# Kernel optimization log

Measured on AMD Instinct MI355X. Metric: run time of the kernel, lower is better.

## Reference

```python
import jax, jax.numpy as jnp
import numpy as np

B = 32; NPG = 290; N = B * NPG; EPG = 2320; E = B * EPG
LP = 900; IN_FEATS = 75; D = 128; HD = 256; K = 3; HK = HD * K; HOUT = 2


def setup_inputs() -> dict:
    key = jax.random.key(0)
    ks = jax.random.split(key, 20)
    s = 0.05
    rng = np.random.default_rng(0)
    off = np.arange(B)[:, None] * NPG  # keep edges inside each graph block
    edge_src = jnp.asarray((rng.integers(0, NPG, (B, EPG)) + off).reshape(-1), dtype=jnp.int32)
    edge_dst = jnp.asarray((rng.integers(0, NPG, (B, EPG)) + off).reshape(-1), dtype=jnp.int32)
    node_h = jax.random.normal(ks[0], (N, IN_FEATS), jnp.float32)
    v_p = jax.random.randint(ks[1], (B, LP), 0, 26, jnp.int32)
    W_init = (jax.random.normal(ks[2], (IN_FEATS, D)) * s).at[:, -1].set(0.0)  # padding unit zeroed
    gcn_W = jax.random.normal(ks[3], (3, 3, D, D)) * s
    gcn_b = jnp.zeros((3, 3, D))
    gcn_Wres = jax.random.normal(ks[4], (3, 3, D, D)) * s
    gcn_bres = jnp.zeros((3, 3, D))
    emb = (jax.random.normal(ks[5], (26, D)) * s).at[0].set(0.0)  # padding_idx=0
    conv1_w = jax.random.normal(ks[6], (D, D, 3)) * s
    conv2_w = jax.random.normal(ks[7], (D, D, 6)) * s
    conv3_w = jax.random.normal(ks[8], (D, D, 9)) * s
    conv_b = jnp.zeros((3, D))
    cnn_bn_g = jnp.ones((3, D)); cnn_bn_b = jnp.zeros((3, D))
    Wv = jax.random.normal(ks[9], (D, HK)) * s; bv = jnp.zeros((HK,))
    Wq = jax.random.normal(ks[10], (D, HK)) * s; bq = jnp.zeros((HK,))
    h_mat = jax.random.normal(ks[11], (HOUT, HK)) * s
    h_bias = jnp.zeros((HOUT,))
    ban_bn_g = jnp.ones((HD,)); ban_bn_b = jnp.zeros((HD,))
    m_w1 = jax.random.normal(ks[12], (HD, 512)) * s; m_b1 = jnp.zeros((512,))
    m_w2 = jax.random.normal(ks[13], (512, 512)) * s; m_b2 = jnp.zeros((512,))
    m_w3 = jax.random.normal(ks[14], (512, 128)) * s; m_b3 = jnp.zeros((128,))
    m_w4 = jax.random.normal(ks[15], (128, 1)) * s; m_b4 = jnp.zeros((1,))
    mbn_g1 = jnp.ones((512,)); mbn_b1 = jnp.zeros((512,))
    mbn_g2 = jnp.ones((512,)); mbn_b2 = jnp.zeros((512,))
    mbn_g3 = jnp.ones((128,)); mbn_b3 = jnp.zeros((128,))
    return dict(node_h=node_h, edge_src=edge_src, edge_dst=edge_dst, v_p=v_p,
                W_init=W_init, gcn_W=gcn_W, gcn_b=gcn_b, gcn_Wres=gcn_Wres, gcn_bres=gcn_bres,
                emb=emb, conv1_w=conv1_w, conv2_w=conv2_w, conv3_w=conv3_w, conv_b=conv_b,
                cnn_bn_g=cnn_bn_g, cnn_bn_b=cnn_bn_b, Wv=Wv, bv=bv, Wq=Wq, bq=bq,
                h_mat=h_mat, h_bias=h_bias, ban_bn_g=ban_bn_g, ban_bn_b=ban_bn_b,
                m_w1=m_w1, m_b1=m_b1, m_w2=m_w2, m_b2=m_b2, m_w3=m_w3, m_b3=m_b3,
                m_w4=m_w4, m_b4=m_b4, mbn_g1=mbn_g1, mbn_b1=mbn_b1, mbn_g2=mbn_g2,
                mbn_b2=mbn_b2, mbn_g3=mbn_g3, mbn_b3=mbn_b3)


def _bn_feat(x, g, b):  # BatchNorm1d on [B, C], training-mode batch stats
    m = jnp.mean(x, 0); v = jnp.var(x, 0)
    return (x - m) * jax.lax.rsqrt(v + 1e-5) * g + b


def _bn_chan(x, g, b):  # BatchNorm1d on [B, C, L]
    m = jnp.mean(x, (0, 2), keepdims=True); v = jnp.var(x, (0, 2), keepdims=True)
    return (x - m) * jax.lax.rsqrt(v + 1e-5) * g[None, :, None] + b[None, :, None]


def _forward(node_h, W_init, gcn_W, gcn_b, gcn_Wres, gcn_bres, emb, conv1_w, conv2_w,
             conv3_w, conv_b, cnn_bn_g, cnn_bn_b, Wv, bv, Wq, bq, h_mat, h_bias,
             ban_bn_g, ban_bn_b, m_w1, m_b1, m_w2, m_b2, m_w3, m_b3, m_w4, m_b4,
             mbn_g1, mbn_b1, mbn_g2, mbn_b2, mbn_g3, mbn_b3, edge_src, edge_dst, v_p):
    relu = jax.nn.relu

    def gcn(h, W, b, Wr, br):  # 3 dgllife GCN layers: sum-aggregate + relu + residual
        for l in range(3):
            agg = jax.ops.segment_sum(h[edge_src], edge_dst, num_segments=N)
            h = relu(agg @ W[l] + b[l]) + relu(h @ Wr[l] + br[l])
        return h

    h0 = node_h @ W_init  # shared init_transform (no bias)
    v_d_o = gcn(h0, gcn_W[0], gcn_b[0], gcn_Wres[0], gcn_bres[0]).reshape(B, NPG, D)
    pos1 = gcn(h0, gcn_W[1], gcn_b[1], gcn_Wres[1], gcn_bres[1]).reshape(B, NPG, D)
    pos2 = gcn(h0, gcn_W[2], gcn_b[2], gcn_Wres[2], gcn_bres[2]).reshape(B, NPG, D)

    x = emb[v_p].transpose(0, 2, 1)  # [B, D, LP]
    dn = ('NCH', 'OIH', 'NCH')
    for w, cb, g, bb in ((conv1_w, conv_b[0], cnn_bn_g[0], cnn_bn_b[0]),
                         (conv2_w, conv_b[1], cnn_bn_g[1], cnn_bn_b[1]),
                         (conv3_w, conv_b[2], cnn_bn_g[2], cnn_bn_b[2])):
        x = jax.lax.conv_general_dilated(x, w, (1,), 'VALID', dimension_numbers=dn) + cb[None, :, None]
        x = _bn_chan(relu(x), g, bb)
    v_p_o = x.transpose(0, 2, 1)  # [B, 885, D]

    q_ = relu(v_p_o @ Wq + bq)  # BAN q_net (shared across views)

    def ban(vd):  # BANLayer forward (eval-mode dropout)
        v_ = relu(vd @ Wv + bv)  # [B, Nv, HK]
        att = jnp.einsum('hk,bvk,bqk->bhvq', h_mat, v_, q_) + h_bias[None, :, None, None]
        f = jnp.einsum('bvk,bhvq,bqk->bk', v_, att, q_)  # summed over h_out heads
        f = f.reshape(-1, HD, K).sum(-1)  # AvgPool1d(k) * k == sum over k groups
        return _bn_feat(f, ban_bn_g, ban_bn_b)

    def mlp(f):
        f = _bn_feat(relu(f @ m_w1 + m_b1), mbn_g1, mbn_b1)
        f = _bn_feat(relu(f @ m_w2 + m_b2), mbn_g2, mbn_b2)
        f = _bn_feat(relu(f @ m_w3 + m_b3), mbn_g3, mbn_b3)
        return f @ m_w4 + m_b4

    f_o = ban(v_d_o)  # Transformer_lar treated as identity -> beta blend is a no-op
    score_o = mlp(f_o)
    s1 = mlp(ban(pos1))
    s2 = mlp(ban(pos2))

    def norm(z):
        return z / jnp.maximum(jnp.linalg.norm(z, axis=1, keepdims=True), 1e-12)

    km = norm(s1) @ norm(s2).T  # cosine_similarity_kernel
    loss = -jnp.mean(jnp.diagonal(jax.nn.log_softmax(km, axis=1)))  # CE vs arange labels
    return jnp.concatenate([score_o, s1, s2, loss * jnp.ones((B, 1), score_o.dtype)], axis=1)


def reference(node_h, edge_src, edge_dst, v_p, W_init, gcn_W, gcn_b, gcn_Wres, gcn_bres,
              emb, conv1_w, conv2_w, conv3_w, conv_b, cnn_bn_g, cnn_bn_b, Wv, bv, Wq, bq,
              h_mat, h_bias, ban_bn_g, ban_bn_b, m_w1, m_b1, m_w2, m_b2, m_w3, m_b3,
              m_w4, m_b4, mbn_g1, mbn_b1, mbn_g2, mbn_b2, mbn_g3, mbn_b3):
    return _forward(node_h, W_init, gcn_W, gcn_b, gcn_Wres, gcn_bres, emb, conv1_w,
                    conv2_w, conv3_w, conv_b, cnn_bn_g, cnn_bn_b, Wv, bv, Wq, bq,
                    h_mat, h_bias, ban_bn_g, ban_bn_b, m_w1, m_b1, m_w2, m_b2, m_w3,
                    m_b3, m_w4, m_b4, mbn_g1, mbn_b1, mbn_g2, mbn_b2, mbn_g3, mbn_b3,
                    edge_src, edge_dst, v_p)
```

## Files before the change

kernel.cpp:

```cpp
#include <hip/hip_runtime.h>
#include <hip/hip_bf16.h>

#define Bc 32
#define NPGc 290
#define Nn 9280
#define Ec 74240
#define LPc 900
#define INFc 75
#define Dd 128
#define HKc 768
#define LQ 885
#define S1 904
#define S2 896
#define S3 888
#define NT 78
#define TSZ 4096

typedef __attribute__((ext_vector_type(8))) short bf16x8;
typedef __attribute__((ext_vector_type(16))) float f32x16;

static __device__ __forceinline__ unsigned short f2bf(float v){
  unsigned int u = __float_as_uint(v);
  unsigned int r = u + 0x7FFFu + ((u >> 16) & 1u);
  return (unsigned short)(r >> 16);
}
static __device__ __forceinline__ float bf2f(unsigned short b){
  return __uint_as_float(((unsigned int)b) << 16);
}

__global__ void k_sentinel(float* out, float val){
  int t = threadIdx.x;
  if (t < 128) out[t] = val;
}

__global__ void k_h0(float* __restrict__ h0, const float* __restrict__ nh, const float* __restrict__ Wi){
  int n = blockIdx.x, j = threadIdx.x;
  __shared__ float arow[INFc];
  if (j < INFc) arow[j] = nh[(size_t)n*INFc + j];
  __syncthreads();
  float s = 0.f;
  #pragma unroll 5
  for (int k=0;k<INFc;k++) s += arow[k]*Wi[(size_t)k*Dd + j];
  h0[(size_t)n*Dd + j] = s;
}

__global__ void k_build_adj(float* __restrict__ A, const int* __restrict__ src, const int* __restrict__ dst){
  int e = blockIdx.x*blockDim.x + threadIdx.x;
  if (e >= Ec) return;
  int s = src[e], d = dst[e];
  int b = d / NPGc;
  int dl = d - b*NPGc, sl = s - b*NPGc;
  atomicAdd(&A[((size_t)b*NPGc + dl)*NPGc + sl], 1.f);
}

__global__ void k_wsplit(unsigned short* __restrict__ dstW, unsigned short* __restrict__ dstWr,
                         const float* __restrict__ W, const float* __restrict__ Wr){
  int idx = blockIdx.x*256 + threadIdx.x;
  if (idx >= 9*Dd*Dd) return;
  int gl = idx >> 14;
  int r  = idx & 16383;
  int k  = r >> 7, j = r & 127;
  int c = k >> 4, slot = k & 15;
  size_t o = ((((size_t)gl*8 + c)*Dd + j) << 4) + slot;
  const size_t NW = (size_t)9*8*Dd*16;
  float v = W[idx];
  unsigned short hi = f2bf(v);
  dstW[o] = hi; dstW[NW + o] = f2bf(v - bf2f(hi));
  float u = Wr[idx];
  unsigned short hr = f2bf(u);
  dstWr[o] = hr; dstWr[NW + o] = f2bf(u - bf2f(hr));
}

__global__ void k_aggm(unsigned short* __restrict__ aggH, unsigned short* __restrict__ aggL,
                       const float* __restrict__ inb, size_t istride,
                       const float* __restrict__ Adj){
  int g = blockIdx.z, b = blockIdx.y;
  int i0 = blockIdx.x*64;
  const float* h = inb + (size_t)g*istride + (size_t)b*NPGc*Dd;
  const float* Ab = Adj + (size_t)b*NPGc*NPGc;
  __shared__ unsigned short Bh[128*24], Bl[128*24];
  int tid = threadIdx.x;
  int w = tid>>6, l = tid&63, lr = l&31, lg = l>>5;
  int mh = w>>1, nh = w&1;
  int kr = tid>>4, jq = tid&15;
  f32x16 acc0={}, acc1={};
  for (int c=0;c<19;c++){
    int k0 = c*16;
    {
      int ci = k0 + kr;
      if (ci < NPGc){
        const float* hr_ = h + (size_t)ci*Dd + jq*8;
        #pragma unroll
        for (int m=0;m<8;m++){
          float v = hr_[m];
          unsigned short hi16 = f2bf(v);
          Bh[(jq*8+m)*24 + kr] = hi16;
          Bl[(jq*8+m)*24 + kr] = f2bf(v - bf2f(hi16));
        }
      } else {
        #pragma unroll
        for (int m=0;m<8;m++){ Bh[(jq*8+m)*24+kr]=0; Bl[(jq*8+m)*24+kr]=0; }
      }
    }
    __syncthreads();
    int row = i0 + mh*32 + lr;
    bf16x8 aA = {0,0,0,0,0,0,0,0};
    if (row < NPGc && k0+15 < NPGc){
      const float* ar_ = Ab + (size_t)row*NPGc + k0 + lg*8;
      #pragma unroll
      for (int m=0;m<8;m++) aA[m] = (short)f2bf(ar_[m]);
    } else if (row < NPGc){
      #pragma unroll
      for (int m=0;m<8;m++){
        int k = k0 + lg*8 + m;
        aA[m] = (short)((k < NPGc) ? f2bf(Ab[(size_t)row*NPGc + k]) : 0);
      }
    }
    bf16x8 b0H = *(const bf16x8*)&Bh[(nh*64+lr)*24 + lg*8];
    bf16x8 b0L = *(const bf16x8*)&Bl[(nh*64+lr)*24 + lg*8];
    bf16x8 b1H = *(const bf16x8*)&Bh[(nh*64+32+lr)*24 + lg*8];
    bf16x8 b1L = *(const bf16x8*)&Bl[(nh*64+32+lr)*24 + lg*8];
    acc0 = __builtin_amdgcn_mfma_f32_32x32x16_bf16(aA, b0H, acc0, 0, 0, 0);
    acc0 = __builtin_amdgcn_mfma_f32_32x32x16_bf16(aA, b0L, acc0, 0, 0, 0);
    acc1 = __builtin_amdgcn_mfma_f32_32x32x16_bf16(aA, b1H, acc1, 0, 0, 0);
    acc1 = __builtin_amdgcn_mfma_f32_32x32x16_bf16(aA, b1L, acc1, 0, 0, 0);
    __syncthreads();
  }
  size_t gb = ((size_t)g*Bc + b)*NPGc;
  int j0 = nh*64 + lr;
  #pragma unroll
  for (int reg=0; reg<16; reg++){
    int rowl = (reg&3) + 8*(reg>>2) + 4*lg;
    int i = i0 + mh*32 + rowl;
    if (i < NPGc){
      size_t base = (gb + i)*Dd;
      float v0 = acc0[reg];
      unsigned short h0_ = f2bf(v0);
      aggH[base + j0] = h0_;
      aggL[base + j0] = f2bf(v0 - bf2f(h0_));
      float v1 = acc1[reg];
      unsigned short h1_ = f2bf(v1);
      aggH[base + j0 + 32] = h1_;
      aggL[base + j0 + 32] = f2bf(v1 - bf2f(h1_));
    }
  }
}

__global__ void k_gcnlin(float* __restrict__ outb, size_t ostride,
                         const unsigned short* __restrict__ aggH, const unsigned short* __restrict__ aggL,
                         const float* __restrict__ inb, size_t istride,
                         const unsigned short* __restrict__ WTs, const unsigned short* __restrict__ WrTs,
                         const float* __restrict__ ball, const float* __restrict__ brall, int lno){
  int g = blockIdx.y;
  int m0 = blockIdx.x*64;
  int gl = g*3 + lno;
  const size_t NW = (size_t)9*8*Dd*16;
  int tid = threadIdx.x;
  int w=tid>>6, l=tid&63, lr=l&31, lg=l>>5;
  int mh=w>>1, nh=w&1;
  const float* hin = inb + (size_t)g*istride;
  const unsigned short* agH = aggH + (size_t)g*Nn*Dd;
  const unsigned short* agL = aggL + (size_t)g*Nn*Dd;
  f32x16 aw0={},aw1={},ar0={},ar1={};
  int row = m0 + mh*32 + lr;
  for (int c=0;c<8;c++){
    int k0 = c*16;
    bf16x8 gH = *(const bf16x8*)&agH[(size_t)row*Dd + k0 + lg*8];
    bf16x8 gL = *(const bf16x8*)&agL[(size_t)row*Dd + k0 + lg*8];
    bf16x8 hH, hL;
    {
      const float* hp = hin + (size_t)row*Dd + k0 + lg*8;
      #pragma unroll
      for (int m=0;m<8;m++){
        float v = hp[m];
        unsigned short x = f2bf(v);
        hH[m] = (short)x;
        hL[m] = (short)f2bf(v - bf2f(x));
      }
    }
    size_t wb0 = ((((size_t)gl*8 + c)*Dd) + nh*64 + lr)*16 + (size_t)lg*8;
    size_t wb1 = wb0 + 32*16;
    bf16x8 w0H = *(const bf16x8*)&WTs[wb0];
    bf16x8 w0L = *(const bf16x8*)&WTs[NW + wb0];
    bf16x8 w1H = *(const bf16x8*)&WTs[wb1];
    bf16x8 w1L = *(const bf16x8*)&WTs[NW + wb1];
    bf16x8 r0H = *(const bf16x8*)&WrTs[wb0];
    bf16x8 r0L = *(const bf16x8*)&WrTs[NW + wb0];
    bf16x8 r1H = *(const bf16x8*)&WrTs[wb1];
    bf16x8 r1L = *(const bf16x8*)&WrTs[NW + wb1];
    aw0 = __builtin_amdgcn_mfma_f32_32x32x16_bf16(gH, w0H, aw0, 0,0,0);
    aw0 = __builtin_amdgcn_mfma_f32_32x32x16_bf16(gH, w0L, aw0, 0,0,0);
    aw0 = __builtin_amdgcn_mfma_f32_32x32x16_bf16(gL, w0H, aw0, 0,0,0);
    aw1 = __builtin_amdgcn_mfma_f32_32x32x16_bf16(gH, w1H, aw1, 0,0,0);
    aw1 = __builtin_amdgcn_mfma_f32_32x32x16_bf16(gH, w1L, aw1, 0,0,0);
    aw1 = __builtin_amdgcn_mfma_f32_32x32x16_bf16(gL, w1H, aw1, 0,0,0);
    ar0 = __builtin_amdgcn_mfma_f32_32x32x16_bf16(hH, r0H, ar0, 0,0,0);
    ar0 = __builtin_amdgcn_mfma_f32_32x32x16_bf16(hH, r0L, ar0, 0,0,0);
    ar0 = __builtin_amdgcn_mfma_f32_32x32x16_bf16(hL, r0H, ar0, 0,0,0);
    ar1 = __builtin_amdgcn_mfma_f32_32x32x16_bf16(hH, r1H, ar1, 0,0,0);
    ar1 = __builtin_amdgcn_mfma_f32_32x32x16_bf16(hH, r1L, ar1, 0,0,0);
    ar1 = __builtin_amdgcn_mfma_f32_32x32x16_bf16(hL, r1H, ar1, 0,0,0);
  }
  float* out = outb + (size_t)g*ostride;
  int j0 = nh*64 + lr;
  float b0 = ball[gl*Dd + j0], b1 = ball[gl*Dd + j0 + 32];
  float c0 = brall[gl*Dd + j0], c1 = brall[gl*Dd + j0 + 32];
  #pragma unroll
  for (int reg=0; reg<16; reg++){
    int rowl = (reg&3)+8*(reg>>2)+4*lg;
    int i = m0 + mh*32 + rowl;
    out[(size_t)i*Dd + j0]      = fmaxf(aw0[reg]+b0,0.f) + fmaxf(ar0[reg]+c0,0.f);
    out[(size_t)i*Dd + j0 + 32] = fmaxf(aw1[reg]+b1,0.f) + fmaxf(ar1[reg]+c1,0.f);
  }
}

__global__ void k_embed(float* __restrict__ x, const int* __restrict__ vp, const float* __restrict__ emb){
  int t = blockIdx.x*blockDim.x + threadIdx.x;
  int d = blockIdx.y, b = blockIdx.z;
  if (t >= LPc) return;
  int tok = vp[b*LPc + t];
  x[((size_t)b*Dd + d)*LPc + t] = emb[(size_t)tok*Dd + d];
}

__global__ void k_wpack16(unsigned short* __restrict__ wp, const float* __restrict__ w,
                          const float* __restrict__ scale, int KW, int C){
  int idx = blockIdx.x*256 + threadIdx.x;
  int tot = C*2048;
  if (idx >= tot) return;
  int c = idx >> 11;
  int r = idx & 2047;
  int o = r >> 4, s = r & 15;
  int k = c*16 + s;
  int i = k / KW, kw = k - i*KW;
  float v = w[((size_t)o*Dd + i)*KW + kw];
  if (scale) v *= scale[i];
  unsigned short hi = f2bf(v);
  wp[idx] = hi;
  wp[(size_t)tot + idx] = f2bf(v - bf2f(hi));
}

__global__ void k_bfold(float* __restrict__ bout, const float* __restrict__ w,
                        const float* __restrict__ shf, const float* __restrict__ cb,
                        int go, int KW){
  int o = blockIdx.x, i = threadIdx.x;
  float p = 0.f;
  if (shf){
    const float* wr = w + ((size_t)o*Dd + i)*KW;
    float s = 0.f;
    for (int kw=0; kw<KW; kw++) s += wr[kw];
    p = s * shf[i];
  }
  __shared__ float red[128];
  red[i] = p; __syncthreads();
  for (int st=64; st>0; st>>=1){
    if (i<st) red[i] += red[i+st];
    __syncthreads();
  }
  if (i==0) bout[o] = cb[go+o] + red[0];
}

template<int KW>
__global__ void k_convmfma2(float* __restrict__ y, const float* __restrict__ x,
                            const unsigned short* __restrict__ wp,
                            const float* __restrict__ biasF,
                            int Lout, int XS, int YS){
  const int C = (Dd*KW)/16;
  int b = blockIdx.y;
  int t0 = blockIdx.x*64;
  __shared__ unsigned short Bh[2][64*24], Bl[2][64*24];
  int tid = threadIdx.x;
  int w = tid>>6, l = tid&63, lr = l&31, lg = l>>5;
  int kx = tid&15, tq = tid>>4;
  const unsigned short* wpL = wp + (size_t)C*2048;
  const float* xb = x + (size_t)b*Dd*XS;
  f32x16 acc0={}, acc1={};
  {
    int i = kx/KW, kw = kx - i*KW;
    const float* xr = xb + (size_t)i*XS + t0 + kw + tq*4;
    #pragma unroll
    for (int j=0;j<4;j++){
      float v = xr[j];
      unsigned short h = f2bf(v);
      Bh[0][(tq*4+j)*24+kx] = h;
      Bl[0][(tq*4+j)*24+kx] = f2bf(v - bf2f(h));
    }
  }
  __syncthreads();
  for (int c=0;c<C;c++){
    int cur = c&1, nxt = cur^1;
    bf16x8 aH = *(const bf16x8*)(wp  + ((size_t)c*128 + w*32+lr)*16 + lg*8);
    bf16x8 aL = *(const bf16x8*)(wpL + ((size_t)c*128 + w*32+lr)*16 + lg*8);
    float pv0=0.f,pv1=0.f,pv2=0.f,pv3=0.f;
    if (c+1<C){
      int k1 = (c+1)*16 + kx;
      int i = k1/KW, kw = k1 - i*KW;
      const float* xr = xb + (size_t)i*XS + t0 + kw + tq*4;
      pv0 = xr[0]; pv1 = xr[1]; pv2 = xr[2]; pv3 = xr[3];
    }
    bf16x8 b0H = *(const bf16x8*)&Bh[cur][lr*24 + lg*8];
    bf16x8 b0L = *(const bf16x8*)&Bl[cur][lr*24 + lg*8];
    bf16x8 b1H = *(const bf16x8*)&Bh[cur][(32+lr)*24 + lg*8];
    bf16x8 b1L = *(const bf16x8*)&Bl[cur][(32+lr)*24 + lg*8];
    acc0 = __builtin_amdgcn_mfma_f32_32x32x16_bf16(aH, b0H, acc0, 0,0,0);
    acc1 = __builtin_amdgcn_mfma_f32_32x32x16_bf16(aH, b1H, acc1, 0,0,0);
    acc0 = __builtin_amdgcn_mfma_f32_32x32x16_bf16(aH, b0L, acc0, 0,0,0);
    acc1 = __builtin_amdgcn_mfma_f32_32x32x16_bf16(aH, b1L, acc1, 0,0,0);
    acc0 = __builtin_amdgcn_mfma_f32_32x32x16_bf16(aL, b0H, acc0, 0,0,0);
    acc1 = __builtin_amdgcn_mfma_f32_32x32x16_bf16(aL, b1H, acc1, 0,0,0);
    if (c+1<C){
      unsigned short h;
      h = f2bf(pv0); Bh[nxt][(tq*4+0)*24+kx]=h; Bl[nxt][(tq*4+0)*24+kx]=f2bf(pv0-bf2f(h));
      h = f2bf(pv1); Bh[nxt][(tq*4+1)*24+kx]=h; Bl[nxt][(tq*4+1)*24+kx]=f2bf(pv1-bf2f(h));
      h = f2bf(pv2); Bh[nxt][(tq*4+2)*24+kx]=h; Bl[nxt][(tq*4+2)*24+kx]=f2bf(pv2-bf2f(h));
      h = f2bf(pv3); Bh[nxt][(tq*4+3)*24+kx]=h; Bl[nxt][(tq*4+3)*24+kx]=f2bf(pv3-bf2f(h));
    }
    __syncthreads();
  }
  int tc = t0 + lr;
  #pragma unroll
  for (int reg=0; reg<16; reg++){
    int row = (reg&3) + 8*(reg>>2) + 4*lg;
    int o = w*32 + row;
    float bias = biasF[o];
    float* yp = y + ((size_t)b*Dd + o)*YS;
    if (tc < Lout)      yp[tc]      = fmaxf(acc0[reg] + bias, 0.f);
    if (tc + 32 < Lout) yp[tc + 32] = fmaxf(acc1[reg] + bias, 0.f);
  }
}

__global__ void k_bnc_stats2(float* __restrict__ scale, float* __restrict__ shift,
                             const float* __restrict__ y, int Lout, int YS,
                             const float* __restrict__ g, const float* __restrict__ bb, int go){
  int c = blockIdx.x;
  float s=0.f, ss=0.f;
  int cnt = Bc*Lout;
  for (int i = threadIdx.x; i < cnt; i += blockDim.x){
    int b = i / Lout, t = i - b*Lout;
    float v = y[((size_t)b*Dd+c)*YS + t];
    s += v; ss += v*v;
  }
  __shared__ float rs[256], rss[256];
  rs[threadIdx.x]=s; rss[threadIdx.x]=ss; __syncthreads();
  for (int st=128; st>0; st>>=1){
    if (threadIdx.x<st){ rs[threadIdx.x]+=rs[threadIdx.x+st]; rss[threadIdx.x]+=rss[threadIdx.x+st]; }
    __syncthreads();
  }
  if (threadIdx.x==0){
    float m = rs[0]/cnt; float v = rss[0]/cnt - m*m; if (v<0.f) v=0.f;
    float r = rsqrtf(v+1e-5f);
    float scl = r*g[go+c];
    scale[c] = scl;
    shift[c] = bb[go+c] - m*scl;
  }
}

__global__ void k_qgemm_tile(unsigned short* __restrict__ qH, unsigned short* __restrict__ qL,
                             const float* __restrict__ x,
                             const float* __restrict__ W, const float* __restrict__ bias,
                             const float* __restrict__ scale, const float* __restrict__ shift,
                             int gbase){
  int bl = blockIdx.z, b = gbase + bl;
  int m0 = blockIdx.y*64;
  int n0 = blockIdx.x*64;
  __shared__ float As[16][64], Bs[16][64];
  int tid = threadIdx.x;
  int tx = tid & 15, ty = tid >> 4;
  int ldr = tid >> 4, ldc = (tid & 15)*4;
  float acc[4][4] = {};
  for (int k0 = 0; k0 < Dd; k0 += 16){
    int d = k0 + ldr;
    float sc_ = scale[d], sh_ = shift[d];
    const float* xrow = x + ((size_t)b*Dd + d)*S3 + m0 + ldc;
    int mb = m0 + ldc;
    float4 a4;
    a4.x = (mb+0 < LQ) ? xrow[0]*sc_+sh_ : 0.f;
    a4.y = (mb+1 < LQ) ? xrow[1]*sc_+sh_ : 0.f;
    a4.z = (mb+2 < LQ) ? xrow[2]*sc_+sh_ : 0.f;
    a4.w = (mb+3 < LQ) ? xrow[3]*sc_+sh_ : 0.f;
    *(float4*)&As[ldr][ldc] = a4;
    *(float4*)&Bs[ldr][ldc] = *(const float4*)(W + (size_t)d*HKc + n0 + ldc);
    __syncthreads();
    #pragma unroll
    for (int kk=0; kk<16; kk++){
      float a[4], bb[4];
      *(float4*)a  = *(const float4*)&As[kk][ty*4];
      *(float4*)bb = *(const float4*)&Bs[kk][tx*4];
      #pragma unroll
      for (int i=0;i<4;i++)
        #pragma unroll
        for (int j=0;j<4;j++) acc[i][j] += a[i]*bb[j];
    }
    __syncthreads();
  }
  #pragma unroll
  for (int i=0;i<4;i++){
    int m = m0 + ty*4 + i;
    if (m >= LQ) continue;
    int n = n0 + tx*4;
    float4 b4 = *(const float4*)(bias + n);
    float o0 = fmaxf(acc[i][0] + b4.x, 0.f);
    float o1 = fmaxf(acc[i][1] + b4.y, 0.f);
    float o2 = fmaxf(acc[i][2] + b4.z, 0.f);
    float o3 = fmaxf(acc[i][3] + b4.w, 0.f);
    ushort4 sh, sl;
    sh.x = f2bf(o0); sl.x = f2bf(o0 - bf2f(sh.x));
    sh.y = f2bf(o1); sl.y = f2bf(o1 - bf2f(sh.y));
    sh.z = f2bf(o2); sl.z = f2bf(o2 - bf2f(sh.z));
    sh.w = f2bf(o3); sl.w = f2bf(o3 - bf2f(sh.w));
    size_t base = ((size_t)bl*LQ + m)*HKc + n;
    *(ushort4*)(qH + base) = sh;
    *(ushort4*)(qL + base) = sl;
  }
}

__global__ void k_colsum_q(float* __restrict__ S, const unsigned short* __restrict__ qH,
                           const unsigned short* __restrict__ qL, int gbase){
  int j = blockIdx.x*256 + threadIdx.x;
  int bl = blockIdx.y;
  if (j >= HKc) return;
  const unsigned short* ph = qH + (size_t)bl*LQ*HKc + j;
  const unsigned short* pl = qL + (size_t)bl*LQ*HKc + j;
  float s=0.f;
  for (int t=0;t<LQ;t++) s += bf2f(ph[(size_t)t*HKc]) + bf2f(pl[(size_t)t*HKc]);
  S[(gbase+bl)*HKc + j] = s;
}

__global__ void k_gram_mfma(float* __restrict__ Gp, const unsigned short* __restrict__ qH,
                            const unsigned short* __restrict__ qL, int gbase){
  int bl = blockIdx.y, bg = gbase + bl;
  int tl0 = blockIdx.x;
  int tl = tl0; int ti = 0;
  while (tl >= 12-ti){ tl -= 12-ti; ti++; }
  int tj = ti + tl;
  int r0 = ti*64, c0 = tj*64;
  const unsigned short* qHb = qH + (size_t)bl*LQ*HKc;
  const unsigned short* qLb = qL + (size_t)bl*LQ*HKc;
  float* Gb = Gp + ((size_t)bg*NT + tl0)*TSZ;
  __shared__ unsigned short Ah[2][64*24], Al[2][64*24], Bh[2][64*24], Bl[2][64*24];
  int tid = threadIdx.x;
  int w = tid>>6, l = tid&63, lr = l&31, lg = l>>5;
  int mi = w>>1, ni = w&1;
  int kr = tid>>4, cg = tid&15;
  const int C = (LQ+15)/16;
  f32x16 acc = {};
  {
    ushort4 z = {0,0,0,0};
    ushort4 ah=z, al=z, bh=z, bl_=z;
    if (kr < LQ){
      const unsigned short* rh = qHb + (size_t)kr*HKc;
      const unsigned short* rl = qLb + (size_t)kr*HKc;
      ah  = *(const ushort4*)(rh + r0 + cg*4);
      al  = *(const ushort4*)(rl + r0 + cg*4);
      bh  = *(const ushort4*)(rh + c0 + cg*4);
      bl_ = *(const ushort4*)(rl + c0 + cg*4);
    }
    int b0 = (cg*4)*24 + kr;
    Ah[0][b0]=ah.x; Ah[0][b0+24]=ah.y; Ah[0][b0+48]=ah.z; Ah[0][b0+72]=ah.w;
    Al[0][b0]=al.x; Al[0][b0+24]=al.y; Al[0][b0+48]=al.z; Al[0][b0+72]=al.w;
    Bh[0][b0]=bh.x; Bh[0][b0+24]=bh.y; Bh[0][b0+48]=bh.z; Bh[0][b0+72]=bh.w;
    Bl[0][b0]=bl_.x; Bl[0][b0+24]=bl_.y; Bl[0][b0+48]=bl_.z; Bl[0][b0+72]=bl_.w;
  }
  __syncthreads();
  for (int c=0;c<C;c++){
    int cur=c&1, nxt=cur^1;
    ushort4 z = {0,0,0,0};
    ushort4 pah=z, pal=z, pbh=z, pbl=z;
    if (c+1<C){
      int t = (c+1)*16 + kr;
      if (t < LQ){
        const unsigned short* rh = qHb + (size_t)t*HKc;
        const unsigned short* rl = qLb + (size_t)t*HKc;
        pah = *(const ushort4*)(rh + r0 + cg*4);
        pal = *(const ushort4*)(rl + r0 + cg*4);
        pbh = *(const ushort4*)(rh + c0 + cg*4);
        pbl = *(const ushort4*)(rl + c0 + cg*4);
      }
    }
    bf16x8 aH = *(const bf16x8*)&Ah[cur][(mi*32+lr)*24 + lg*8];
    bf16x8 aL = *(const bf16x8*)&Al[cur][(mi*32+lr)*24 + lg*8];
    bf16x8 bH = *(const bf16x8*)&Bh[cur][(ni*32+lr)*24 + lg*8];
    bf16x8 bL = *(const bf16x8*)&Bl[cur][(ni*32+lr)*24 + lg*8];
    acc = __builtin_amdgcn_mfma_f32_32x32x16_bf16(aH, bH, acc, 0,0,0);
    acc = __builtin_amdgcn_mfma_f32_32x32x16_bf16(aH, bL, acc, 0,0,0);
    acc = __builtin_amdgcn_mfma_f32_32x32x16_bf16(aL, bH, acc, 0,0,0);
    if (c+1<C){
      int b0 = (cg*4)*24 + kr;
      Ah[nxt][b0]=pah.x; Ah[nxt][b0+24]=pah.y; Ah[nxt][b0+48]=pah.z; Ah[nxt][b0+72]=pah.w;
      Al[nxt][b0]=pal.x; Al[nxt][b0+24]=pal.y; Al[nxt][b0+48]=pal.z; Al[nxt][b0+72]=pal.w;
      Bh[nxt][b0]=pbh.x; Bh[nxt][b0+24]=pbh.y; Bh[nxt][b0+48]=pbh.z; Bh[nxt][b0+72]=pbh.w;
      Bl[nxt][b0]=pbl.x; Bl[nxt][b0+24]=pbl.y; Bl[nxt][b0+48]=pbl.z; Bl[nxt][b0+72]=pbl.w;
    }
    __syncthreads();
  }
  #pragma unroll
  for (int reg=0; reg<16; reg++){
    int row = (reg&3) + 8*(reg>>2) + 4*lg;
    Gb[(size_t)(mi*32+row)*64 + ni*32 + lr] = acc[reg];
  }
}

__global__ void k_vgemm8(float* __restrict__ v, const float* __restrict__ vd,
                         const float* __restrict__ W, const float* __restrict__ bias){
  int j = blockIdx.x*256 + threadIdx.x;
  int r0 = blockIdx.y*8;
  __shared__ float xr[8][Dd];
  for (int idx=threadIdx.x; idx<8*Dd; idx+=256){
    int r = idx>>7, k = idx&127;
    xr[r][k] = vd[(size_t)(r0 + r)*Dd + k];
  }
  __syncthreads();
  float acc[8];
  float bj = bias[j];
  #pragma unroll
  for (int r=0;r<8;r++) acc[r]=bj;
  for (int k=0;k<Dd;k++){
    float wk = W[(size_t)k*HKc+j];
    #pragma unroll
    for (int r=0;r<8;r++) acc[r] += xr[r][k]*wk;
  }
  #pragma unroll
  for (int r=0;r<8;r++)
    v[(size_t)(r0+r)*HKc + j] = fmaxf(acc[r],0.f);
}

__global__ void k_colsum_v(float* __restrict__ S, const float* __restrict__ X){
  int j = blockIdx.x*blockDim.x + threadIdx.x;
  int bl = blockIdx.y;
  if (j >= HKc) return;
  const float* p = X + (size_t)bl*NPGc*HKc + j;
  float s=0.f;
  for (int t=0;t<NPGc;t++) s += p[(size_t)t*HKc];
  S[bl*HKc + j] = s;
}

__global__ void k_gramf_sym(float* __restrict__ f, const float* __restrict__ V,
                            const float* __restrict__ Gp, const float* __restrict__ hm){
  int bg = blockIdx.z;
  int tl0 = blockIdx.x;
  int tl = tl0; int ti = 0;
  while (tl >= 12-ti){ tl -= 12-ti; ti++; }
  int tj = ti + tl;
  int r0 = ti*64, c0 = tj*64;
  int offdiag = (ti != tj);
  const float* Vb = V + (size_t)bg*NPGc*HKc;
  __shared__ float As[16][64], Bs[16][64];
  __shared__ float wc[64], wr[64];
  int tid = threadIdx.x;
  int tx = tid & 15, ty = tid >> 4;
  int ldr = tid >> 4, ldc = (tid & 15)*4;
  if (tid < 64) wc[tid] = hm[c0+tid] + hm[HKc + c0 + tid];
  else if (tid < 128) wr[tid-64] = hm[r0+tid-64] + hm[HKc + r0 + tid-64];
  float acc[4][4] = {};
  for (int t0=0; t0<NPGc; t0+=16){
    float4 av = make_float4(0.f,0.f,0.f,0.f), bv4 = make_float4(0.f,0.f,0.f,0.f);
    if (t0+ldr < NPGc){
      const float* row = Vb + (size_t)(t0+ldr)*HKc;
      av  = *(const float4*)(row + r0 + ldc);
      bv4 = *(const float4*)(row + c0 + ldc);
    }
    *(float4*)&As[ldr][ldc] = av;
    *(float4*)&Bs[ldr][ldc] = bv4;
    __syncthreads();
    #pragma unroll
    for (int tt=0; tt<16; tt++){
      float a[4], bb[4];
      *(float4*)a  = *(const float4*)&As[tt][ty*4];
      *(float4*)bb = *(const float4*)&Bs[tt][tx*4];
      #pragma unroll
      for (int i=0;i<4;i++)
        #pragma unroll
        for (int j=0;j<4;j++) acc[i][j] += a[i]*bb[j];
    }
    __syncthreads();
  }
  const float* gqb = Gp + ((size_t)bg*NT + tl0)*TSZ;
  float w0 = wc[tx*4+0], w1 = wc[tx*4+1], w2 = wc[tx*4+2], w3 = wc[tx*4+3];
  float colp[4] = {0.f,0.f,0.f,0.f};
  #pragma unroll
  for (int i=0;i<4;i++){
    int rl = ty*4 + i;
    int r = r0 + rl;
    const float4 g4 = *(const float4*)(gqb + rl*64 + tx*4);
    float s = acc[i][0]*w0*g4.x + acc[i][1]*w1*g4.y
            + acc[i][2]*w2*g4.z + acc[i][3]*w3*g4.w;
    s += __shfl_xor(s, 1); s += __shfl_xor(s, 2);
    s += __shfl_xor(s, 4); s += __shfl_xor(s, 8);
    if (tx==0) atomicAdd(&f[bg*HKc + r], s);
    if (offdiag){
      float wri = wr[rl];
      colp[0] += acc[i][0]*wri*g4.x;
      colp[1] += acc[i][1]*wri*g4.y;
      colp[2] += acc[i][2]*wri*g4.z;
      colp[3] += acc[i][3]*wri*g4.w;
    }
  }
  if (offdiag){
    #pragma unroll
    for (int j=0;j<4;j++){
      colp[j] += __shfl_xor(colp[j], 16);
      colp[j] += __shfl_xor(colp[j], 32);
    }
    if ((tid & 48) == 0){
      #pragma unroll
      for (int j=0;j<4;j++)
        atomicAdd(&f[bg*HKc + c0 + tx*4 + j], colp[j]);
    }
  }
}

__global__ void k_pool3(float* __restrict__ fp, const float* __restrict__ f3,
                        const float* __restrict__ Sv3, const float* __restrict__ Sq,
                        const float* __restrict__ hb){
  int idx = blockIdx.x*256 + threadIdx.x;
  if (idx >= 3*Bc*256) return;
  int v = idx >> 13;
  int rem = idx & 8191;
  int b = rem >> 8, c = rem & 255;
  const float* f = f3 + (size_t)v*Bc*HKc;
  const float* Sv = Sv3 + (size_t)v*Bc*HKc;
  float hbs = hb[0] + hb[1];
  float s = 0.f;
  #pragma unroll
  for (int r=0;r<3;r++){
    int k = c*3 + r;
    s += f[b*HKc + k] + hbs*Sv[b*HKc + k]*Sq[b*HKc + k];
  }
  fp[idx] = s;
}

__global__ void k_bnfeat3(float* __restrict__ y, const float* __restrict__ x, const float* __restrict__ g,
                          const float* __restrict__ bb, int C){
  int c = blockIdx.x; int v = blockIdx.y; int b = threadIdx.x;
  __shared__ float buf[32];
  __shared__ float mv[2];
  int row = v*32 + b;
  float val = x[(size_t)row*C + c];
  buf[b] = val;
  __syncthreads();
  if (b == 0){
    float s = 0.f;
    for (int i=0;i<32;i++) s += buf[i];
    float m = s/32.f;
    float vs = 0.f;
    for (int i=0;i<32;i++){ float d = buf[i]-m; vs += d*d; }
    mv[0] = m; mv[1] = vs/32.f;
  }
  __syncthreads();
  y[(size_t)row*C + c] = (val - mv[0])*rsqrtf(mv[1]+1e-5f)*g[c] + bb[c];
}

__global__ void k_mlp(float* __restrict__ out, const float* __restrict__ in, const float* __restrict__ W,
                      const float* __restrict__ bias, int K, int Nc, int doRelu){
  int b = blockIdx.y;
  int j = blockIdx.x*blockDim.x + threadIdx.x;
  __shared__ float xr[512];
  for (int k=threadIdx.x; k<K; k+=blockDim.x) xr[k] = in[(size_t)b*K+k];
  __syncthreads();
  if (j >= Nc) return;
  float s = bias[j];
  for (int k=0;k<K;k++) s += xr[k]*W[(size_t)k*Nc + j];
  if (doRelu) s = fmaxf(s, 0.f);
  out[(size_t)b*Nc + j] = s;
}

__global__ void k_score96(float* __restrict__ sc, const float* __restrict__ h, const float* __restrict__ w,
                          const float* __restrict__ bb){
  int b = threadIdx.x; if (b>=96) return;
  float s = bb[0];
  for (int k=0;k<Dd;k++) s += h[(size_t)b*Dd+k]*w[k];
  sc[b] = s;
}

__global__ void k_out(float* __restrict__ out, const float* __restrict__ scores){
  int t = threadIdx.x;
  __shared__ float loss_s;
  if (t == 0){
    float sn1[32], sn2[32];
    for (int i=0;i<32;i++){
      float a = scores[32+i]; sn1[i] = a / fmaxf(fabsf(a), 1e-12f);
      float c = scores[64+i]; sn2[i] = c / fmaxf(fabsf(c), 1e-12f);
    }
    float acc = 0.f;
    for (int i=0;i<32;i++){
      float mx = -1e30f;
      for (int j=0;j<32;j++) mx = fmaxf(mx, sn1[i]*sn2[j]);
      float se = 0.f;
      for (int j=0;j<32;j++) se += expf(sn1[i]*sn2[j]-mx);
      acc += sn1[i]*sn2[i] - (mx + logf(se));
    }
    loss_s = -acc/32.f;
  }
  __syncthreads();
  out[t*4+0] = scores[t];
  out[t*4+1] = scores[32+t];
  out[t*4+2] = scores[64+t];
  out[t*4+3] = loss_s;
}

extern "C" void kernel_launch(void* const* d_in, const int* in_sizes, int n_in,
                              void* d_out, int out_size, void* d_ws, size_t ws_size,
                              hipStream_t stream){
  static const int exp_sizes[38] = {
    Nn*INFc, Ec, Ec, Bc*LPc, INFc*Dd,
    9*Dd*Dd, 9*Dd, 9*Dd*Dd, 9*Dd,
    26*Dd, Dd*Dd*3, Dd*Dd*6, Dd*Dd*9, 3*Dd, 3*Dd, 3*Dd,
    Dd*HKc, HKc, Dd*HKc, HKc, 2*HKc, 2, 256, 256,
    256*512, 512, 512*512, 512, 512*128, 128, 128, 1,
    512, 512, 512, 512, 128, 128 };
  if (n_in != 38){ k_sentinel<<<1,128,0,stream>>>((float*)d_out, 2000.f + n_in); return; }
  for (int i=0;i<38;i++){
    if (in_sizes[i] != exp_sizes[i]){
      k_sentinel<<<1,128,0,stream>>>((float*)d_out, 1000.f + i); return;
    }
  }

  const float* node_h=(const float*)d_in[0];
  const int*  esrc  =(const int*)d_in[1];
  const int*  edst  =(const int*)d_in[2];
  const int*  vp    =(const int*)d_in[3];
  const float* W_init=(const float*)d_in[4];
  const float* gcn_W =(const float*)d_in[5];
  const float* gcn_b =(const float*)d_in[6];
  const float* gcn_Wr=(const float*)d_in[7];
  const float* gcn_br=(const float*)d_in[8];
  const float* emb   =(const float*)d_in[9];
  const float* c1w=(const float*)d_in[10];
  const float* c2w=(const float*)d_in[11];
  const float* c3w=(const float*)d_in[12];
  const float* cbv=(const float*)d_in[13];
  const float* bng=(const float*)d_in[14];
  const float* bnb=(const float*)d_in[15];
  const float* Wv =(const float*)d_in[16];
  const float* bvv=(const float*)d_in[17];
  const float* Wq =(const float*)d_in[18];
  const float* bq =(const float*)d_in[19];
  const float* hmat =(const float*)d_in[20];
  const float* hbias=(const float*)d_in[21];
  const float* bang =(const float*)d_in[22];
  const float* banb =(const float*)d_in[23];
  const float* mw1=(const float*)d_in[24]; const float* mb1=(const float*)d_in[25];
  const float* mw2=(const float*)d_in[26]; const float* mb2=(const float*)d_in[27];
  const float* mw3=(const float*)d_in[28]; const float* mb3=(const float*)d_in[29];
  const float* mw4=(const float*)d_in[30]; const float* mb4=(const float*)d_in[31];
  const float* g1=(const float*)d_in[32]; const float* bb1=(const float*)d_in[33];
  const float* g2=(const float*)d_in[34]; const float* bb2=(const float*)d_in[35];
  const float* g3=(const float*)d_in[36]; const float* bb3=(const float*)d_in[37];

  float* ws = (float*)d_ws;
  size_t off = 0;
  auto alloc = [&](size_t n){ float* p = ws + off; off += n; return p; };

  const size_t NDsz = (size_t)Nn*Dd;
  const size_t CNNBP = (size_t)Bc*Dd*S1;
  const size_t ADJ  = (size_t)Bc*NPGc*NPGc;
  const size_t QB8  = (size_t)8*LQ*HKc;
  const size_t VB   = (size_t)Bc*NPGc*HKc;
  const size_t AGGF = (size_t)3*Nn*Dd;
  size_t ARENA = 7*NDsz + ADJ + AGGF;
  if (ARENA < 4*NDsz + VB) ARENA = 4*NDsz + VB;
  if (ARENA < CNNBP + QB8) ARENA = CNNBP + QB8;
  if (ARENA < 2*CNNBP) ARENA = 2*CNNBP;

  float* Sq   = alloc((size_t)Bc*HKc);
  float* Sv3  = alloc((size_t)3*Bc*HKc);
  float* fbuf3= alloc((size_t)3*Bc*HKc);
  float* fpool3=alloc((size_t)3*Bc*256);
  float* hh1  = alloc((size_t)96*512);
  float* hh2  = alloc((size_t)96*512);
  float* hh3  = alloc((size_t)96*128);
  float* sc   = alloc(96);
  float* scl1 = alloc(128); float* shf1 = alloc(128);
  float* scl2 = alloc(128); float* shf2 = alloc(128);
  float* scl3 = alloc(128); float* shf3 = alloc(128);
  float* b1f  = alloc(128); float* b2f  = alloc(128); float* b3f = alloc(128);
  unsigned short* wp1 = (unsigned short*)alloc((size_t)384*128);
  unsigned short* wp2 = (unsigned short*)alloc((size_t)768*128);
  unsigned short* wp3 = (unsigned short*)alloc((size_t)1152*128);
  unsigned short* WTs  = (unsigned short*)alloc(147456);
  unsigned short* WrTs = (unsigned short*)alloc(147456);
  float* Gqp = alloc((size_t)Bc*NT*TSZ);
  float* arena = alloc(ARENA);

  float* cnnA = arena;
  float* cnnB = arena + CNNBP;
  float* qbuf = arena + CNNBP;
  unsigned short* qH = (unsigned short*)qbuf;
  unsigned short* qL = qH + (size_t)8*LQ*HKc;
  float* h0b  = arena;
  float* Bb   = arena + NDsz;
  float* Cb   = arena + 4*NDsz;
  float* Adj  = arena + 7*NDsz;
  unsigned short* aggH = (unsigned short*)(arena + 7*NDsz + ADJ);
  unsigned short* aggL = aggH + (size_t)3*Nn*Dd;
  float* vbuf = arena + 4*NDsz;

  k_wpack16<<<(24*2048+255)/256,256,0,stream>>>(wp1, c1w, nullptr, 3, 24);
  k_bfold<<<128,128,0,stream>>>(b1f, c1w, nullptr, cbv, 0, 3);
  k_wsplit<<<(9*Dd*Dd+255)/256,256,0,stream>>>(WTs, WrTs, gcn_W, gcn_Wr);

  k_embed<<<dim3((LPc+127)/128, Dd, Bc),128,0,stream>>>(cnnB, vp, emb);
  k_convmfma2<3><<<dim3(15,Bc),256,0,stream>>>(cnnA, cnnB, wp1, b1f, 898, 900, S1);
  k_bnc_stats2<<<Dd,256,0,stream>>>(scl1, shf1, cnnA, 898, S1, bng, bnb, 0);
  k_wpack16<<<(48*2048+255)/256,256,0,stream>>>(wp2, c2w, scl1, 6, 48);
  k_bfold<<<128,128,0,stream>>>(b2f, c2w, shf1, cbv, 128, 6);
  k_convmfma2<6><<<dim3(14,Bc),256,0,stream>>>(cnnB, cnnA, wp2, b2f, 893, S1, S2);
  k_bnc_stats2<<<Dd,256,0,stream>>>(scl2, shf2, cnnB, 893, S2, bng, bnb, 128);
  k_wpack16<<<(72*2048+255)/256,256,0,stream>>>(wp3, c3w, scl2, 9, 72);
  k_bfold<<<128,128,0,stream>>>(b3f, c3w, shf2, cbv, 256, 9);
  k_convmfma2<9><<<dim3(14,Bc),256,0,stream>>>(cnnA, cnnB, wp3, b3f, 885, S2, S3);
  k_bnc_stats2<<<Dd,256,0,stream>>>(scl3, shf3, cnnA, 885, S3, bng, bnb, 256);

  for (int gb = 0; gb < Bc; gb += 8){
    k_qgemm_tile<<<dim3(12,(LQ+63)/64,8),256,0,stream>>>(qH, qL, cnnA, Wq, bq, scl3, shf3, gb);
    k_colsum_q<<<dim3(3,8),256,0,stream>>>(Sq, qH, qL, gb);
    k_gram_mfma<<<dim3(NT,8),256,0,stream>>>(Gqp, qH, qL, gb);
  }

  hipMemsetAsync(Adj, 0, ADJ*sizeof(float), stream);
  k_build_adj<<<(Ec+255)/256,256,0,stream>>>(Adj, esrc, edst);

  hipMemsetAsync(fbuf3, 0, (size_t)3*Bc*HKc*sizeof(float), stream);

  k_h0<<<Nn,Dd,0,stream>>>(h0b, node_h, W_init);
  k_aggm<<<dim3(5,Bc,3),256,0,stream>>>(aggH, aggL, h0b, 0, Adj);
  k_gcnlin<<<dim3(145,3),256,0,stream>>>(Bb, NDsz, aggH, aggL, h0b, 0, WTs, WrTs, gcn_b, gcn_br, 0);
  k_aggm<<<dim3(5,Bc,3),256,0,stream>>>(aggH, aggL, Bb, NDsz, Adj);
  k_gcnlin<<<dim3(145,3),256,0,stream>>>(Cb, NDsz, aggH, aggL, Bb, NDsz, WTs, WrTs, gcn_b, gcn_br, 1);
  k_aggm<<<dim3(5,Bc,3),256,0,stream>>>(aggH, aggL, Cb, NDsz, Adj);
  k_gcnlin<<<dim3(145,3),256,0,stream>>>(Bb, NDsz, aggH, aggL, Cb, NDsz, WTs, WrTs, gcn_b, gcn_br, 2);

  for (int g=0; g<3; g++){
    k_vgemm8<<<dim3(3,(Bc*NPGc)/8),256,0,stream>>>(vbuf, Bb + (size_t)g*NDsz, Wv, bvv);
    k_colsum_v<<<dim3(3,Bc),256,0,stream>>>(Sv3 + (size_t)g*Bc*HKc, vbuf);
    k_gramf_sym<<<dim3(NT,1,Bc),256,0,stream>>>(fbuf3 + (size_t)g*Bc*HKc, vbuf, Gqp, hmat);
  }

  k_pool3<<<(3*Bc*256+255)/256,256,0,stream>>>(fpool3, fbuf3, Sv3, Sq, hbias);
  k_bnfeat3<<<dim3(256,3),32,0,stream>>>(fpool3, fpool3, bang, banb, 256);
  k_mlp<<<dim3(2,96),256,0,stream>>>(hh1, fpool3, mw1, mb1, 256, 512, 1);
  k_bnfeat3<<<dim3(512,3),32,0,stream>>>(hh1, hh1, g1, bb1, 512);
  k_mlp<<<dim3(2,96),256,0,stream>>>(hh2, hh1, mw2, mb2, 512, 512, 1);
  k_bnfeat3<<<dim3(512,3),32,0,stream>>>(hh2, hh2, g2, bb2, 512);
  k_mlp<<<dim3(1,96),256,0,stream>>>(hh3, hh2, mw3, mb3, 512, 128, 1);
  k_bnfeat3<<<dim3(128,3),32,0,stream>>>(hh3, hh3, g3, bb3, 128);
  k_score96<<<1,96,0,stream>>>(sc, hh3, mw4, mb4);
  k_out<<<1,32,0,stream>>>((float*)d_out, sc);
}
```

Before: 2.017 ms.

## Store q transposed and padded so gram MFMA loads operands directly

The q-projection GEMM now writes its bf16 hi/lo split outputs transposed (feature-major, token dimension padded to 896 with zeros). The gram kernel then loads MFMA operand fragments straight from global memory with contiguous 16-byte loads, dropping the LDS double-buffer staging and barriers. The column-sum kernel reads contiguous ushort4 rows instead of strided columns. In exchange, the GEMM epilogue writes are strided across rows and gram operand reads rely on cache rather than shared-memory reuse.

```diff
diff --git a/kernel.cpp b/kernel.cpp
--- a/kernel.cpp
+++ b/kernel.cpp
@@ -10,6 +10,7 @@
 #define Dd 128
 #define HKc 768
 #define LQ 885
+#define LQP 896
 #define S1 904
 #define S2 896
 #define S3 888
@@ -354,7 +355,7 @@
   }
 }
 
-__global__ void k_qgemm_tile(unsigned short* __restrict__ qH, unsigned short* __restrict__ qL,
+__global__ void k_qgemm_tile(unsigned short* __restrict__ qTH, unsigned short* __restrict__ qTL,
                              const float* __restrict__ x,
                              const float* __restrict__ W, const float* __restrict__ bias,
                              const float* __restrict__ scale, const float* __restrict__ shift,
@@ -393,104 +394,72 @@
     __syncthreads();
   }
   #pragma unroll
-  for (int i=0;i<4;i++){
-    int m = m0 + ty*4 + i;
-    if (m >= LQ) continue;
-    int n = n0 + tx*4;
-    float4 b4 = *(const float4*)(bias + n);
-    float o0 = fmaxf(acc[i][0] + b4.x, 0.f);
-    float o1 = fmaxf(acc[i][1] + b4.y, 0.f);
-    float o2 = fmaxf(acc[i][2] + b4.z, 0.f);
-    float o3 = fmaxf(acc[i][3] + b4.w, 0.f);
+  for (int j2=0;j2<4;j2++){
+    int n = n0 + tx*4 + j2;
+    float bn = bias[n];
     ushort4 sh, sl;
-    sh.x = f2bf(o0); sl.x = f2bf(o0 - bf2f(sh.x));
-    sh.y = f2bf(o1); sl.y = f2bf(o1 - bf2f(sh.y));
-    sh.z = f2bf(o2); sl.z = f2bf(o2 - bf2f(sh.z));
-    sh.w = f2bf(o3); sl.w = f2bf(o3 - bf2f(sh.w));
-    size_t base = ((size_t)bl*LQ + m)*HKc + n;
-    *(ushort4*)(qH + base) = sh;
-    *(ushort4*)(qL + base) = sl;
-  }
-}
-
-__global__ void k_colsum_q(float* __restrict__ S, const unsigned short* __restrict__ qH,
-                           const unsigned short* __restrict__ qL, int gbase){
+    unsigned short hv[4], lv[4];
+    #pragma unroll
+    for (int i2=0;i2<4;i2++){
+      int m = m0 + ty*4 + i2;
+      float v = (m < LQ) ? fmaxf(acc[i2][j2] + bn, 0.f) : 0.f;
+      unsigned short h = f2bf(v);
+      hv[i2] = h; lv[i2] = f2bf(v - bf2f(h));
+    }
+    sh.x=hv[0]; sh.y=hv[1]; sh.z=hv[2]; sh.w=hv[3];
+    sl.x=lv[0]; sl.y=lv[1]; sl.z=lv[2]; sl.w=lv[3];
+    size_t base = ((size_t)bl*HKc + n)*LQP + m0 + ty*4;
+    *(ushort4*)(qTH + base) = sh;
+    *(ushort4*)(qTL + base) = sl;
+  }
+}
+
+__global__ void k_colsum_qT(float* __restrict__ S, const unsigned short* __restrict__ qTH,
+                            const unsigned short* __restrict__ qTL, int gbase){
   int j = blockIdx.x*256 + threadIdx.x;
   int bl = blockIdx.y;
   if (j >= HKc) return;
-  const unsigned short* ph = qH + (size_t)bl*LQ*HKc + j;
-  const unsigned short* pl = qL + (size_t)bl*LQ*HKc + j;
+  const ushort4* ph = (const ushort4*)(qTH + ((size_t)bl*HKc + j)*LQP);
+  const ushort4* pl = (const ushort4*)(qTL + ((size_t)bl*HKc + j)*LQP);
   float s=0.f;
-  for (int t=0;t<LQ;t++) s += bf2f(ph[(size_t)t*HKc]) + bf2f(pl[(size_t)t*HKc]);
+  for (int t=0;t<LQP/4;t++){
+    ushort4 a = ph[t], c = pl[t];
+    s += bf2f(a.x)+bf2f(a.y)+bf2f(a.z)+bf2f(a.w);
+    s += bf2f(c.x)+bf2f(c.y)+bf2f(c.z)+bf2f(c.w);
+  }
   S[(gbase+bl)*HKc + j] = s;
 }
 
-__global__ void k_gram_mfma(float* __restrict__ Gp, const unsigned short* __restrict__ qH,
-                            const unsigned short* __restrict__ qL, int gbase){
-  int bl = blockIdx.y, bg = gbase + bl;
-  int tl0 = blockIdx.x;
+__global__ void k_gramT(float* __restrict__ Gp, const unsigned short* __restrict__ qTH,
+                        const unsigned short* __restrict__ qTL, int gbase){
+  int blk = blockIdx.x;
+  int bl = blk & 7;
+  int tl0 = blk >> 3;
+  int bg = gbase + bl;
   int tl = tl0; int ti = 0;
   while (tl >= 12-ti){ tl -= 12-ti; ti++; }
   int tj = ti + tl;
   int r0 = ti*64, c0 = tj*64;
-  const unsigned short* qHb = qH + (size_t)bl*LQ*HKc;
-  const unsigned short* qLb = qL + (size_t)bl*LQ*HKc;
+  const unsigned short* qH = qTH + (size_t)bl*HKc*LQP;
+  const unsigned short* qL = qTL + (size_t)bl*HKc*LQP;
   float* Gb = Gp + ((size_t)bg*NT + tl0)*TSZ;
-  __shared__ unsigned short Ah[2][64*24], Al[2][64*24], Bh[2][64*24], Bl[2][64*24];
   int tid = threadIdx.x;
   int w = tid>>6, l = tid&63, lr = l&31, lg = l>>5;
   int mi = w>>1, ni = w&1;
-  int kr = tid>>4, cg = tid&15;
-  const int C = (LQ+15)/16;
+  const unsigned short* aHp = qH + (size_t)(r0 + mi*32 + lr)*LQP + lg*8;
+  const unsigned short* aLp = qL + (size_t)(r0 + mi*32 + lr)*LQP + lg*8;
+  const unsigned short* bHp = qH + (size_t)(c0 + ni*32 + lr)*LQP + lg*8;
+  const unsigned short* bLp = qL + (size_t)(c0 + ni*32 + lr)*LQP + lg*8;
   f32x16 acc = {};
-  {
-    ushort4 z = {0,0,0,0};
-    ushort4 ah=z, al=z, bh=z, bl_=z;
-    if (kr < LQ){
-      const unsigned short* rh = qHb + (size_t)kr*HKc;
-      const unsigned short* rl = qLb + (size_t)kr*HKc;
-      ah  = *(const ushort4*)(rh + r0 + cg*4);
-      al  = *(const ushort4*)(rl + r0 + cg*4);
-      bh  = *(const ushort4*)(rh + c0 + cg*4);
-      bl_ = *(const ushort4*)(rl + c0 + cg*4);
-    }
-    int b0 = (cg*4)*24 + kr;
-    Ah[0][b0]=ah.x; Ah[0][b0+24]=ah.y; Ah[0][b0+48]=ah.z; Ah[0][b0+72]=ah.w;
-    Al[0][b0]=al.x; Al[0][b0+24]=al.y; Al[0][b0+48]=al.z; Al[0][b0+72]=al.w;
-    Bh[0][b0]=bh.x; Bh[0][b0+24]=bh.y; Bh[0][b0+48]=bh.z; Bh[0][b0+72]=bh.w;
-    Bl[0][b0]=bl_.x; Bl[0][b0+24]=bl_.y; Bl[0][b0+48]=bl_.z; Bl[0][b0+72]=bl_.w;
-  }
-  __syncthreads();
-  for (int c=0;c<C;c++){
-    int cur=c&1, nxt=cur^1;
-    ushort4 z = {0,0,0,0};
-    ushort4 pah=z, pal=z, pbh=z, pbl=z;
-    if (c+1<C){
-      int t = (c+1)*16 + kr;
-      if (t < LQ){
-        const unsigned short* rh = qHb + (size_t)t*HKc;
-        const unsigned short* rl = qLb + (size_t)t*HKc;
-        pah = *(const ushort4*)(rh + r0 + cg*4);
-        pal = *(const ushort4*)(rl + r0 + cg*4);
-        pbh = *(const ushort4*)(rh + c0 + cg*4);
-        pbl = *(const ushort4*)(rl + c0 + cg*4);
-      }
-    }
-    bf16x8 aH = *(const bf16x8*)&Ah[cur][(mi*32+lr)*24 + lg*8];
-    bf16x8 aL = *(const bf16x8*)&Al[cur][(mi*32+lr)*24 + lg*8];
-    bf16x8 bH = *(const bf16x8*)&Bh[cur][(ni*32+lr)*24 + lg*8];
-    bf16x8 bL = *(const bf16x8*)&Bl[cur][(ni*32+lr)*24 + lg*8];
+  #pragma unroll 4
+  for (int c=0;c<LQP/16;c++){
+    bf16x8 aH = *(const bf16x8*)(aHp + c*16);
+    bf16x8 aL = *(const bf16x8*)(aLp + c*16);
+    bf16x8 bH = *(const bf16x8*)(bHp + c*16);
+    bf16x8 bL = *(const bf16x8*)(bLp + c*16);
     acc = __builtin_amdgcn_mfma_f32_32x32x16_bf16(aH, bH, acc, 0,0,0);
     acc = __builtin_amdgcn_mfma_f32_32x32x16_bf16(aH, bL, acc, 0,0,0);
     acc = __builtin_amdgcn_mfma_f32_32x32x16_bf16(aL, bH, acc, 0,0,0);
-    if (c+1<C){
-      int b0 = (cg*4)*24 + kr;
-      Ah[nxt][b0]=pah.x; Ah[nxt][b0+24]=pah.y; Ah[nxt][b0+48]=pah.z; Ah[nxt][b0+72]=pah.w;
-      Al[nxt][b0]=pal.x; Al[nxt][b0+24]=pal.y; Al[nxt][b0+48]=pal.z; Al[nxt][b0+72]=pal.w;
-      Bh[nxt][b0]=pbh.x; Bh[nxt][b0+24]=pbh.y; Bh[nxt][b0+48]=pbh.z; Bh[nxt][b0+72]=pbh.w;
-      Bl[nxt][b0]=pbl.x; Bl[nxt][b0+24]=pbl.y; Bl[nxt][b0+48]=pbl.z; Bl[nxt][b0+72]=pbl.w;
-    }
-    __syncthreads();
   }
   #pragma unroll
   for (int reg=0; reg<16; reg++){
@@ -753,12 +722,12 @@
   const size_t NDsz = (size_t)Nn*Dd;
   const size_t CNNBP = (size_t)Bc*Dd*S1;
   const size_t ADJ  = (size_t)Bc*NPGc*NPGc;
-  const size_t QB8  = (size_t)8*LQ*HKc;
+  const size_t QTF  = (size_t)8*HKc*LQP;
   const size_t VB   = (size_t)Bc*NPGc*HKc;
   const size_t AGGF = (size_t)3*Nn*Dd;
   size_t ARENA = 7*NDsz + ADJ + AGGF;
   if (ARENA < 4*NDsz + VB) ARENA = 4*NDsz + VB;
-  if (ARENA < CNNBP + QB8) ARENA = CNNBP + QB8;
+  if (ARENA < CNNBP + QTF) ARENA = CNNBP + QTF;
   if (ARENA < 2*CNNBP) ARENA = 2*CNNBP;
 
   float* Sq   = alloc((size_t)Bc*HKc);
@@ -784,8 +753,8 @@
   float* cnnA = arena;
   float* cnnB = arena + CNNBP;
   float* qbuf = arena + CNNBP;
-  unsigned short* qH = (unsigned short*)qbuf;
-  unsigned short* qL = qH + (size_t)8*LQ*HKc;
+  unsigned short* qTH = (unsigned short*)qbuf;
+  unsigned short* qTL = qTH + (size_t)8*HKc*LQP;
   float* h0b  = arena;
   float* Bb   = arena + NDsz;
   float* Cb   = arena + 4*NDsz;
@@ -811,9 +780,9 @@
   k_bnc_stats2<<<Dd,256,0,stream>>>(scl3, shf3, cnnA, 885, S3, bng, bnb, 256);
 
   for (int gb = 0; gb < Bc; gb += 8){
-    k_qgemm_tile<<<dim3(12,(LQ+63)/64,8),256,0,stream>>>(qH, qL, cnnA, Wq, bq, scl3, shf3, gb);
-    k_colsum_q<<<dim3(3,8),256,0,stream>>>(Sq, qH, qL, gb);
-    k_gram_mfma<<<dim3(NT,8),256,0,stream>>>(Gqp, qH, qL, gb);
+    k_qgemm_tile<<<dim3(12,LQP/64,8),256,0,stream>>>(qTH, qTL, cnnA, Wq, bq, scl3, shf3, gb);
+    k_colsum_qT<<<dim3(3,8),256,0,stream>>>(Sq, qTH, qTL, gb);
+    k_gramT<<<NT*8,256,0,stream>>>(Gqp, qTH, qTL, gb);
   }
 
   hipMemsetAsync(Adj, 0, ADJ*sizeof(float), stream);
```

New measurement: 1.763 ms. -12.6%, faster.
